# Performance work log

Hardware: AMD Instinct MI355X
Metric: run time of the kernel (lower is better)

The kernel has to match this reference:

```python
import jax, jax.numpy as jnp
import numpy as np

N_UNITS = 512
N_HEADS = 8
CHUNK = N_UNITS // N_HEADS
SCALE = 1.0 / (CHUNK ** 0.5)


def setup_inputs() -> dict:
    key = jax.random.key(0)
    k1, k2, k3, k4, k5, k6 = jax.random.split(key, 6)
    B, Nx, Ny = 8, 1024, 1024
    x = jax.random.normal(k1, (B, N_UNITS, Nx), dtype=jnp.float32)
    y = jax.random.normal(k2, (B, N_UNITS, Ny), dtype=jnp.float32)
    xy_mask = jax.random.randint(k3, (B, Nx, Ny), 0, 2) > 0
    # conv1x1 weight [out, in] (ConvolutionSentence, bias=False)
    W = jax.random.normal(k4, (N_UNITS, N_UNITS), dtype=jnp.float32) * (1.0 / np.sqrt(N_UNITS))
    fc_w = jax.random.normal(k5, (1, N_HEADS), dtype=jnp.float32) * (1.0 / np.sqrt(N_HEADS))
    fc_b = jax.random.normal(k6, (1,), dtype=jnp.float32) * 0.01
    return {"x": x, "y": y, "xy_mask": xy_mask, "W": W, "fc_w": fc_w, "fc_b": fc_b}


def reference(x, y, xy_mask, W, fc_w, fc_b):
    B, U, Nx = x.shape
    Ny = y.shape[2]
    H, C = N_HEADS, CHUNK
    # 1x1 conv over channel dim == linear on channels
    _x = jnp.einsum('oi,bin->bon', W, x)  # [B, U, Nx]
    _y = jnp.einsum('oi,bim->bom', W, y)  # [B, U, Ny]
    # split channels into heads (contiguous chunks, matching torch.split)
    xh = _x.reshape(B, H, C, Nx)
    yh = _y.reshape(B, H, C, Ny)
    # per-head scores: relu, then scale, then mask (order matches torch code)
    s = jnp.einsum('bhcn,bhcm->bhnm', xh, yh)  # [B, H, Nx, Ny]
    s = jnp.maximum(s, 0.0) * SCALE
    s = jnp.where(xy_mask[:, None, :, :], s, 0.0)
    similarity = s.sum(axis=(2, 3))  # [B, H]
    n_el = xy_mask.sum(axis=(1, 2))
    n_el = jnp.where(n_el == 0, 1, n_el).astype(similarity.dtype)
    expectation = similarity / n_el[:, None]
    return expectation @ fc_w.T + fc_b  # [B, 1]
```

## Files before the change

### kernel.cpp

```cpp
#include <hip/hip_runtime.h>
#include <stdint.h>

#define UU 512
#define NHEAD 8
#define NB 8
#define NXX 1024
#define NYY 1024
#define SCALE_F 0.125f

typedef __bf16 bf16x8 __attribute__((ext_vector_type(8)));
typedef float f32x4 __attribute__((ext_vector_type(4)));
typedef unsigned short us4 __attribute__((ext_vector_type(4)));

__device__ __forceinline__ unsigned short f2bf(float f) {
  union { float f; uint32_t u; } v; v.f = f;
  return (unsigned short)((v.u + 0x7FFFu + ((v.u >> 16) & 1u)) >> 16);
}

__global__ void prep_kernel(const float* __restrict__ W, unsigned short* __restrict__ Wb,
                            const unsigned char* __restrict__ m, int* __restrict__ det) {
  int blk = blockIdx.x, t = threadIdx.x;
  if (blk < 1024) {
    int i = blk * 256 + t;
    Wb[i] = f2bf(W[i]);
  } else {
    int idx = ((blk - 1024) * 256 + t) * 16;
    uint4 v = *(const uint4*)(m + idx);
    unsigned int c1 = (v.x & 0xff00u) | (v.y & 0xff00u) | (v.z & 0xff00u) | (v.w & 0xff00u);
    if (c1) atomicOr(&det[0], 1);
  }
}

__global__ __launch_bounds__(256, 2) void conv_fused(
    const float* __restrict__ x, const float* __restrict__ y,
    const unsigned short* __restrict__ Wb, unsigned short* __restrict__ cv) {
  __shared__ unsigned short bs[32 * 512];
  int fl = blockIdx.x;
  int bz = fl & 15, nt = fl >> 4;
  int b = bz & 7;
  const float* src = (bz >> 3) ? y : x;
  int n0 = nt * 32;
  int t = threadIdx.x;

  {
    int cq = (t & 7) * 4;
    int i2b = (t >> 3) * 2;
    const float* gb = src + (size_t)b * UU * NXX + n0 + cq;
#pragma unroll
    for (int it = 0; it < 8; it++) {
      int i2 = i2b + it * 64;
      float4 va = *(const float4*)(gb + (size_t)i2 * NXX);
      float4 vb = *(const float4*)(gb + (size_t)(i2 + 1) * NXX);
#pragma unroll
      for (int j = 0; j < 4; j++) {
        int n = cq + j;
        unsigned int pk = (unsigned int)f2bf(((const float*)&va)[j])
                        | ((unsigned int)f2bf(((const float*)&vb)[j]) << 16);
        int e = n * 512 + (i2 ^ ((n & 7) << 3));
        *(unsigned int*)&bs[e] = pk;
      }
    }
  }
  __syncthreads();

  int w = t >> 6, l = t & 63;
  int lane_m = l & 15, lane_g = l >> 4;
  int u0 = w * 128;
  f32x4 acc[2][8] = {};
  bf16x8 aA[8], aB[8], bA[2], bB[2];

#define LOADW(Adst, Bdst, KB) do {                                            \
    int k_ = (KB) * 32 + lane_g * 8;                                          \
    _Pragma("unroll") for (int tu = 0; tu < 8; tu++)                          \
      Adst[tu] = *(const bf16x8*)(Wb + (size_t)(u0 + tu * 16 + lane_m) * UU + k_); \
    _Pragma("unroll") for (int tn = 0; tn < 2; tn++) {                        \
      int nl_ = tn * 16 + lane_m;                                             \
      Bdst[tn] = *(const bf16x8*)&bs[nl_ * 512 + (k_ ^ ((nl_ & 7) << 3))];    \
    }                                                                         \
  } while (0)
#define DOMFMA(Ab, Bb) do {                                                   \
    _Pragma("unroll") for (int tn = 0; tn < 2; tn++)                          \
    _Pragma("unroll") for (int tu = 0; tu < 8; tu++)                          \
      acc[tn][tu] = __builtin_amdgcn_mfma_f32_16x16x32_bf16(Ab[tu], Bb[tn], acc[tn][tu], 0, 0, 0); \
  } while (0)

  LOADW(aA, bA, 0);
#pragma unroll
  for (int kp = 0; kp < 8; kp++) {
    LOADW(aB, bB, 2 * kp + 1);
    DOMFMA(aA, bA);
    if (kp < 7) LOADW(aA, bA, 2 * kp + 2);
    DOMFMA(aB, bB);
  }
#undef LOADW
#undef DOMFMA

  unsigned short* ob = cv + (size_t)bz * NXX * UU;
#pragma unroll
  for (int tn = 0; tn < 2; tn++)
#pragma unroll
    for (int tu = 0; tu < 8; tu++) {
      int n = n0 + tn * 16 + lane_m;
      int u = u0 + tu * 16 + 4 * lane_g;
      us4 pk;
      pk.x = f2bf(acc[tn][tu][0]); pk.y = f2bf(acc[tn][tu][1]);
      pk.z = f2bf(acc[tn][tu][2]); pk.w = f2bf(acc[tn][tu][3]);
      *(us4*)(ob + (size_t)n * UU + u) = pk;
    }
}

__global__ __launch_bounds__(256, 2) void score_kernel(
    const unsigned short* __restrict__ cv, const void* __restrict__ maskp,
    const int* __restrict__ det, float* __restrict__ part) {
  __shared__ unsigned short ys[64 * 512];
  __shared__ unsigned short mf16[64][72];
  __shared__ float red[4][8];
  int fl = blockIdx.x;
  int b = fl & 7, rr = fl >> 3;
  int nt = rr & 15, mt = rr >> 4;
  int t = threadIdx.x, w = t >> 6, l = t & 63;
  int lane_m = l & 15, lane_g = l >> 4;
  int n0 = nt * 64, m0 = mt * 64;
  int nw0 = (w & 1) * 32, hq = (w >> 1) * 4;

  const unsigned short* xb = cv + ((size_t)b * NXX + n0 + nw0) * UU;
  bf16x8 afr[4][2][2];
#pragma unroll
  for (int hh = 0; hh < 4; hh++) {
    int co = (hq + hh) * 64;
#pragma unroll
    for (int tn = 0; tn < 2; tn++)
#pragma unroll
      for (int kb = 0; kb < 2; kb++)
        afr[hh][tn][kb] = *(const bf16x8*)(xb + (size_t)(tn * 16 + lane_m) * UU + co + kb * 32 + lane_g * 8);
  }

  const unsigned short* yb = cv + ((size_t)(NB + b) * NYY + m0) * UU;
  {
    int seg = t & 63;
#pragma unroll
    for (int p = 0; p < 16; p++) {
      int r2 = p * 4 + (t >> 6);
      uint4 v = *(const uint4*)(yb + (size_t)r2 * UU + seg * 8);
      int sp = seg ^ (r2 & 7);
      *(uint4*)&ys[r2 * 512 + sp * 8] = v;
    }
  }

  int is_u8 = det[0] != 0;
  unsigned int cl = 0;
  {
    int row = t >> 2, cq = (t & 3) * 16;
    size_t eb = ((size_t)b * NXX + n0 + row) * NYY + m0 + cq;
    if (is_u8) {
      uint4 v = *(const uint4*)((const unsigned char*)maskp + eb);
#pragma unroll
      for (int j = 0; j < 16; j++) {
        unsigned int word = ((const unsigned int*)&v)[j >> 2];
        int bit = ((word >> ((j & 3) * 8)) & 0xffu) != 0;
        mf16[row][cq + j] = bit ? 0x3F80u : 0u;
        cl += (unsigned)bit;
      }
    } else {
      const unsigned int* mp = (const unsigned int*)maskp + eb;
#pragma unroll
      for (int q = 0; q < 4; q++) {
        uint4 v = *(const uint4*)(mp + q * 4);
        unsigned int wds[4] = {v.x, v.y, v.z, v.w};
#pragma unroll
        for (int j = 0; j < 4; j++) {
          int bit = wds[j] != 0;
          mf16[row][cq + q * 4 + j] = bit ? 0x3F80u : 0u;
          cl += (unsigned)bit;
        }
      }
    }
  }
  for (int s = 1; s < 64; s <<= 1) cl += __shfl_xor(cl, s);
  if (l == 0) red[w][4] = (float)cl;
  __syncthreads();

  float mreg[2][4][4];
#pragma unroll
  for (int tn = 0; tn < 2; tn++)
#pragma unroll
    for (int tm = 0; tm < 4; tm++)
#pragma unroll
      for (int r = 0; r < 4; r++) {
        unsigned int u = (unsigned int)mf16[nw0 + tn * 16 + 4 * lane_g + r][tm * 16 + lane_m] << 16;
        union { unsigned int u; float f; } cvt; cvt.u = u;
        mreg[tn][tm][r] = cvt.f;
      }

  float hsv[4] = {0.f, 0.f, 0.f, 0.f};
#pragma unroll
  for (int hh = 0; hh < 4; hh++) {
    int segbase = (hq + hh) * 8;
    bf16x8 bfr[4][2];
#pragma unroll
    for (int tm = 0; tm < 4; tm++) {
      int row = tm * 16 + lane_m;
#pragma unroll
      for (int kb = 0; kb < 2; kb++) {
        int sp = (segbase + kb * 4 + lane_g) ^ (row & 7);
        bfr[tm][kb] = *(const bf16x8*)&ys[row * 512 + sp * 8];
      }
    }
#pragma unroll
    for (int tn = 0; tn < 2; tn++)
#pragma unroll
      for (int tm = 0; tm < 4; tm++) {
        f32x4 acc = {};
        acc = __builtin_amdgcn_mfma_f32_16x16x32_bf16(afr[hh][tn][0], bfr[tm][0], acc, 0, 0, 0);
        acc = __builtin_amdgcn_mfma_f32_16x16x32_bf16(afr[hh][tn][1], bfr[tm][1], acc, 0, 0, 0);
#pragma unroll
        for (int r = 0; r < 4; r++) {
          float v = acc[r];
          v = v > 0.f ? v : 0.f;
          hsv[hh] = fmaf(v, mreg[tn][tm][r], hsv[hh]);
        }
      }
  }
#pragma unroll
  for (int hh = 0; hh < 4; hh++) {
    float hs = hsv[hh];
    for (int s = 1; s < 64; s <<= 1) hs += __shfl_xor(hs, s);
    if (l == 0) red[w][hh] = hs;
  }
  __syncthreads();
  float* pb = part + (size_t)fl * 16;
  if (t < 8) {
    int q = t >> 2, hh = t & 3;
    pb[t] = red[q * 2][hh] + red[q * 2 + 1][hh];
  } else if (t == 8) {
    pb[8] = red[0][4] + red[1][4] + red[2][4] + red[3][4];
  }
}

__global__ __launch_bounds__(256) void finalize(
    const float* __restrict__ part, const float* __restrict__ fcw,
    const float* __restrict__ fcb, float* __restrict__ out) {
  __shared__ float red[4][9];
  int b = blockIdx.x;
  int t = threadIdx.x, w = t >> 6, l = t & 63;
  const float* pb = part + (size_t)(t * 8 + b) * 16;
  float v[9];
#pragma unroll
  for (int j = 0; j < 9; j++) v[j] = pb[j];
#pragma unroll
  for (int j = 0; j < 9; j++) {
    float s = v[j];
    for (int ss = 1; ss < 64; ss <<= 1) s += __shfl_xor(s, ss);
    v[j] = s;
  }
  if (l == 0)
#pragma unroll
    for (int j = 0; j < 9; j++) red[w][j] = v[j];
  __syncthreads();
  if (t == 0) {
    float s = 0.f, cn = 0.f;
#pragma unroll
    for (int h = 0; h < NHEAD; h++)
      s += (red[0][h] + red[1][h] + red[2][h] + red[3][h]) * fcw[h];
    cn = red[0][8] + red[1][8] + red[2][8] + red[3][8];
    if (cn < 0.5f) cn = 1.f;
    out[b] = s * (SCALE_F / cn) + fcb[0];
  }
}

extern "C" void kernel_launch(void* const* d_in, const int* in_sizes, int n_in,
                              void* d_out, int out_size, void* d_ws, size_t ws_size,
                              hipStream_t stream) {
  const float* x = (const float*)d_in[0];
  const float* y = (const float*)d_in[1];
  const void* mask = d_in[2];
  const float* W = (const float*)d_in[3];
  const float* fcw = (const float*)d_in[4];
  const float* fcb = (const float*)d_in[5];
  float* out = (float*)d_out;
  char* ws = (char*)d_ws;

  unsigned short* cv = (unsigned short*)ws;
  unsigned short* Wb = (unsigned short*)(ws + (16u << 20));
  float* part = (float*)(ws + (16u << 20) + (1u << 19));
  char* st = ws + (16u << 20) + (1u << 19) + (1u << 17);
  int* det = (int*)st;

  hipMemsetAsync(st, 0, 64, stream);
  prep_kernel<<<1040, 256, 0, stream>>>(W, Wb, (const unsigned char*)mask, det);
  conv_fused<<<512, 256, 0, stream>>>(x, y, Wb, cv);
  score_kernel<<<2048, 256, 0, stream>>>(cv, mask, det, part);
  finalize<<<NB, 256, 0, stream>>>(part, fcw, fcb, out);
}
```

Before: 166.1 us.

## Stage W tiles through swizzled LDS and split conv output channels across blocks

The conv kernel now splits the 512 output channels into two halves across blocks, doubling the grid to 1024. Weight tiles of 256x64 are staged through a swizzled LDS buffer with register prefetch of the next k-tile, replacing direct per-wave global loads of W fragments. This cuts redundant global/L2 traffic for W and lowers accumulator register pressure. In exchange, each block converts the same x tile twice and adds two barriers per k-step.

```diff
diff --git a/kernel.cpp b/kernel.cpp
--- a/kernel.cpp
+++ b/kernel.cpp
@@ -34,13 +34,15 @@
 __global__ __launch_bounds__(256, 2) void conv_fused(
     const float* __restrict__ x, const float* __restrict__ y,
     const unsigned short* __restrict__ Wb, unsigned short* __restrict__ cv) {
-  __shared__ unsigned short bs[32 * 512];
+  __shared__ unsigned short xs[32 * 512];
+  __shared__ unsigned short wsld[256 * 64];
   int fl = blockIdx.x;
-  int bz = fl & 15, nt = fl >> 4;
+  int bz = fl & 15, nt = (fl >> 4) & 31, ut = fl >> 9;
   int b = bz & 7;
   const float* src = (bz >> 3) ? y : x;
   int n0 = nt * 32;
-  int t = threadIdx.x;
+  int t = threadIdx.x, w = t >> 6, l = t & 63;
+  int lane_m = l & 15, lane_g = l >> 4;
 
   {
     int cq = (t & 7) * 4;
@@ -57,51 +59,76 @@
         unsigned int pk = (unsigned int)f2bf(((const float*)&va)[j])
                         | ((unsigned int)f2bf(((const float*)&vb)[j]) << 16);
         int e = n * 512 + (i2 ^ ((n & 7) << 3));
-        *(unsigned int*)&bs[e] = pk;
-      }
-    }
-  }
+        *(unsigned int*)&xs[e] = pk;
+      }
+    }
+  }
+
+  int u_l[8], gsl[8];
+#pragma unroll
+  for (int j = 0; j < 8; j++) {
+    int chunk = j * 4 + w;
+    u_l[j] = chunk * 8 + (l >> 3);
+    gsl[j] = (l & 7) ^ (u_l[j] & 7);
+  }
+  const unsigned short* wsrc = Wb + (size_t)ut * 256 * UU + (l & 7) * 8;
+  uint4 wreg[8];
+
+#define ISSUEW(KT) do {                                                       \
+    _Pragma("unroll") for (int j = 0; j < 8; j++)                             \
+      wreg[j] = *(const uint4*)(wsrc + (size_t)u_l[j] * UU + (KT) * 64);      \
+  } while (0)
+#define WRITEW() do {                                                         \
+    _Pragma("unroll") for (int j = 0; j < 8; j++)                             \
+      *(uint4*)&wsld[u_l[j] * 64 + gsl[j] * 8] = wreg[j];                     \
+  } while (0)
+
+  f32x4 acc[2][4] = {};
+  ISSUEW(0);
+  WRITEW();
   __syncthreads();
 
-  int w = t >> 6, l = t & 63;
-  int lane_m = l & 15, lane_g = l >> 4;
-  int u0 = w * 128;
-  f32x4 acc[2][8] = {};
-  bf16x8 aA[8], aB[8], bA[2], bB[2];
-
-#define LOADW(Adst, Bdst, KB) do {                                            \
-    int k_ = (KB) * 32 + lane_g * 8;                                          \
-    _Pragma("unroll") for (int tu = 0; tu < 8; tu++)                          \
-      Adst[tu] = *(const bf16x8*)(Wb + (size_t)(u0 + tu * 16 + lane_m) * UU + k_); \
-    _Pragma("unroll") for (int tn = 0; tn < 2; tn++) {                        \
-      int nl_ = tn * 16 + lane_m;                                             \
-      Bdst[tn] = *(const bf16x8*)&bs[nl_ * 512 + (k_ ^ ((nl_ & 7) << 3))];    \
-    }                                                                         \
-  } while (0)
-#define DOMFMA(Ab, Bb) do {                                                   \
-    _Pragma("unroll") for (int tn = 0; tn < 2; tn++)                          \
-    _Pragma("unroll") for (int tu = 0; tu < 8; tu++)                          \
-      acc[tn][tu] = __builtin_amdgcn_mfma_f32_16x16x32_bf16(Ab[tu], Bb[tn], acc[tn][tu], 0, 0, 0); \
-  } while (0)
-
-  LOADW(aA, bA, 0);
-#pragma unroll
-  for (int kp = 0; kp < 8; kp++) {
-    LOADW(aB, bB, 2 * kp + 1);
-    DOMFMA(aA, bA);
-    if (kp < 7) LOADW(aA, bA, 2 * kp + 2);
-    DOMFMA(aB, bB);
-  }
-#undef LOADW
-#undef DOMFMA
+  for (int kt = 0; kt < 8; kt++) {
+    if (kt < 7) ISSUEW(kt + 1);
+    bf16x8 af[2][4], bff[2][2];
+#pragma unroll
+    for (int kb = 0; kb < 2; kb++) {
+#pragma unroll
+      for (int tu = 0; tu < 4; tu++) {
+        int ur = w * 64 + tu * 16 + lane_m;
+        int gp = ((kb * 4 + lane_g) ^ (ur & 7)) * 8;
+        af[kb][tu] = *(const bf16x8*)&wsld[ur * 64 + gp];
+      }
+#pragma unroll
+      for (int tn = 0; tn < 2; tn++) {
+        int nl = tn * 16 + lane_m;
+        int ka = kt * 64 + kb * 32 + lane_g * 8;
+        bff[kb][tn] = *(const bf16x8*)&xs[nl * 512 + (ka ^ ((nl & 7) << 3))];
+      }
+    }
+#pragma unroll
+    for (int kb = 0; kb < 2; kb++)
+#pragma unroll
+      for (int tn = 0; tn < 2; tn++)
+#pragma unroll
+        for (int tu = 0; tu < 4; tu++)
+          acc[tn][tu] = __builtin_amdgcn_mfma_f32_16x16x32_bf16(af[kb][tu], bff[kb][tn], acc[tn][tu], 0, 0, 0);
+    __syncthreads();
+    if (kt < 7) {
+      WRITEW();
+      __syncthreads();
+    }
+  }
+#undef ISSUEW
+#undef WRITEW
 
   unsigned short* ob = cv + (size_t)bz * NXX * UU;
 #pragma unroll
   for (int tn = 0; tn < 2; tn++)
 #pragma unroll
-    for (int tu = 0; tu < 8; tu++) {
+    for (int tu = 0; tu < 4; tu++) {
       int n = n0 + tn * 16 + lane_m;
-      int u = u0 + tu * 16 + 4 * lane_g;
+      int u = ut * 256 + w * 64 + tu * 16 + 4 * lane_g;
       us4 pk;
       pk.x = f2bf(acc[tn][tu][0]); pk.y = f2bf(acc[tn][tu][1]);
       pk.z = f2bf(acc[tn][tu][2]); pk.w = f2bf(acc[tn][tu][3]);
@@ -288,7 +315,7 @@
 
   hipMemsetAsync(st, 0, 64, stream);
   prep_kernel<<<1040, 256, 0, stream>>>(W, Wb, (const unsigned char*)mask, det);
-  conv_fused<<<512, 256, 0, stream>>>(x, y, Wb, cv);
+  conv_fused<<<1024, 256, 0, stream>>>(x, y, Wb, cv);
   score_kernel<<<2048, 256, 0, stream>>>(cv, mask, det, part);
   finalize<<<NB, 256, 0, stream>>>(part, fcw, fcb, out);
 }
```

Result: slower. 208.4 us (+25.5%).
